# Performance work log

Hardware: AMD Instinct MI355X
Metric: run time of the kernel (lower is better)

## Reference

```python
import jax, jax.numpy as jnp
import numpy as np

TEMPERATURE = 0.07
B, D, NUM_CLASSES = 8192, 256, 100

def setup_inputs() -> dict:
    key = jax.random.key(0)
    kz, kl = jax.random.split(key)
    z = jax.random.normal(kz, (B, D), dtype=jnp.float32)
    z = z / jnp.linalg.norm(z, axis=-1, keepdims=True)  # unit-norm embeddings keep exp(logits/T) finite
    labels = jax.random.randint(kl, (B,), 0, NUM_CLASSES, dtype=jnp.int64)
    return {"z": z, "labels": labels}

def reference(z, labels):
    n = z.shape[0]
    same = labels[:, None] == labels[None, :]              # [B, B] bool
    eye = jnp.eye(n, dtype=bool)
    pos_mask = (same & ~eye).astype(z.dtype)               # positives exclude self
    neg_mask = (~same).astype(z.dtype)                     # mask == 0 entries
    exp_logits = jnp.exp(z @ z.T / TEMPERATURE)            # [B, B]
    sum_neg = jnp.sum(exp_logits * neg_mask, axis=1)       # [B]
    # per positive pair: -log(e_ij / (e_ij + sum_neg_i))
    pair_loss = jnp.log1p(sum_neg[:, None] / exp_logits)   # = -log(e/(e+sn)), stable form
    pos_cnt = jnp.sum(pos_mask, axis=1)                    # [B]
    row_loss = jnp.sum(pair_loss * pos_mask, axis=1) / jnp.maximum(pos_cnt, 1.0)
    valid = (pos_cnt > 0).astype(z.dtype)
    n_valid = jnp.sum(valid)
    loss = jnp.where(n_valid > 0,
                     jnp.sum(row_loss * valid) / jnp.maximum(n_valid, 1.0),
                     jnp.zeros((), z.dtype))
    return loss
```

## Files before the change

kernel.cpp:

```cpp
#include <hip/hip_runtime.h>
#include <hip/hip_bf16.h>


#define BN 8192
#define DD 256
#define INV_T (1.0f / 0.07f)
#define CAPI 256
#define CAP 160

typedef __attribute__((ext_vector_type(8))) __bf16 bf16x8;
typedef __attribute__((ext_vector_type(4))) float f32x4;

typedef const __attribute__((address_space(1))) void gas_void;
typedef __attribute__((address_space(3))) void las_void;

static __device__ __forceinline__ void gld_lds16(const void* g, void* l) {
    __builtin_amdgcn_global_load_lds((gas_void*)g, (las_void*)l, 16, 0, 0);
}

static __device__ __forceinline__ unsigned short f2bf(float f) {
    unsigned int u = __builtin_bit_cast(unsigned int, f);
    u = (u + 0x7FFFu + ((u >> 16) & 1u)) >> 16;
    return (unsigned short)u;
}

__global__ __launch_bounds__(256) void k_prep(const float* __restrict__ z,
                                              unsigned short* __restrict__ zbf,
                                              const int* __restrict__ labels,
                                              int* __restrict__ cls_cnt,
                                              int* __restrict__ cls_idx) {
    const int gid = blockIdx.x * 256 + threadIdx.x;
    const float4* z4 = (const float4*)z;
    float4 v0 = z4[gid * 2 + 0];
    float4 v1 = z4[gid * 2 + 1];
    unsigned short r[8];
    r[0] = f2bf(v0.x); r[1] = f2bf(v0.y); r[2] = f2bf(v0.z); r[3] = f2bf(v0.w);
    r[4] = f2bf(v1.x); r[5] = f2bf(v1.y); r[6] = f2bf(v1.z); r[7] = f2bf(v1.w);
    ((uint4*)zbf)[gid] = *(const uint4*)r;
    if (gid < BN) {
        const int c = labels[gid];
        const int slot = atomicAdd(&cls_cnt[c], 1);
        if (slot < CAPI) cls_idx[c * CAPI + slot] = gid;
    }
}

__global__ __launch_bounds__(512, 2) void k_passA(const unsigned short* __restrict__ zbf,
                                                  float* __restrict__ sn_part) {
    __shared__ char Bb[2][65536];
    __shared__ float sn_lds[128];

    const int tid = threadIdx.x;
    const int w = tid >> 6, lane = tid & 63;
    const int l15 = lane & 15, lk = lane >> 4;
    const int wr = w & 1, wc = w >> 1;
    const int by = blockIdx.x >> 2;
    const int cq = blockIdx.x & 3;
    const int rowbase = by * 128;
    const int colbase = cq * 2048;
    const char* zb = (const char*)zbf;

    auto stage = [&](int buf, int ns) {
        const char* gB = zb + ((size_t)(colbase + ns * 128)) * 512;
        char* lb = Bb[buf];
#pragma unroll
        for (int qq = 0; qq < 8; ++qq) {
            const int s = (qq * 512 + tid) * 16;
            const int col = s >> 9, koff = s & 511;
            gld_lds16(gB + (size_t)col * 512 + (koff ^ ((col & 7) << 4)), lb + s);
        }
    };

    {
        const char* gA = zb + (size_t)rowbase * 512;
#pragma unroll
        for (int qq = 0; qq < 8; ++qq) {
            const int s = (qq * 512 + tid) * 16;
            const int row = s >> 9, koff = s & 511;
            gld_lds16(gA + (size_t)row * 512 + (koff ^ ((row & 7) << 4)),
                      (char*)Bb[0] + s);
        }
    }
    __syncthreads();

    bf16x8 a[4][8];
#pragma unroll
    for (int m = 0; m < 4; ++m) {
        const int row = wr * 64 + m * 16 + l15;
        const int sw = (row & 7) << 4;
#pragma unroll
        for (int kf = 0; kf < 8; ++kf)
            a[m][kf] = *(const bf16x8*)(Bb[0] + row * 512 + ((lk * 16 + kf * 64) ^ sw));
    }
    if (tid < 128) sn_lds[tid] = 0.f;
    float snp[4][4] = {};
    __syncthreads();

    stage(0, 0);
    stage(1, 1);
    asm volatile("s_waitcnt vmcnt(8)" ::: "memory");
    __builtin_amdgcn_s_barrier();
    __builtin_amdgcn_sched_barrier(0);

    for (int ns = 0; ns < 16; ++ns) {
        const int buf = ns & 1;
        const char* bp0 = Bb[buf];
        f32x4 acc[2][4];

#pragma unroll
        for (int n = 0; n < 2; ++n) {
            const int colL = wc * 32 + n * 16 + l15;
            const char* bp = bp0 + (size_t)colL * 512;
            const int sw = (colL & 7) << 4;
            bf16x8 b[8];
#pragma unroll
            for (int kf = 0; kf < 8; ++kf)
                b[kf] = *(const bf16x8*)(bp + ((lk * 16 + kf * 64) ^ sw));
#pragma unroll
            for (int m = 0; m < 4; ++m) acc[n][m] = (f32x4){0.f, 0.f, 0.f, 0.f};
            __builtin_amdgcn_s_setprio(1);
#pragma unroll
            for (int kf = 0; kf < 8; ++kf)
#pragma unroll
                for (int m = 0; m < 4; ++m)
                    acc[n][m] = __builtin_amdgcn_mfma_f32_16x16x32_bf16(a[m][kf], b[kf], acc[n][m], 0, 0, 0);
            __builtin_amdgcn_s_setprio(0);
        }

        __builtin_amdgcn_sched_barrier(0);
        __builtin_amdgcn_s_barrier();
        if (ns + 2 < 16) stage(buf, ns + 2);

#pragma unroll
        for (int n = 0; n < 2; ++n) {
            const int jj = colbase + ns * 128 + wc * 32 + n * 16 + l15;
#pragma unroll
            for (int m = 0; m < 4; ++m) {
                const int ig = rowbase + wr * 64 + m * 16 + lk * 4;
#pragma unroll
                for (int rr = 0; rr < 4; ++rr) {
                    float e = __expf(acc[n][m][rr] * INV_T);
                    if (ig + rr == jj) e = 0.f;
                    snp[m][rr] += e;
                }
            }
        }

        if (ns + 2 < 16) {
            asm volatile("s_waitcnt vmcnt(8)" ::: "memory");
        } else {
            asm volatile("s_waitcnt vmcnt(0)" ::: "memory");
        }
        __builtin_amdgcn_s_barrier();
        __builtin_amdgcn_sched_barrier(0);
    }

#pragma unroll
    for (int m = 0; m < 4; ++m) {
#pragma unroll
        for (int rr = 0; rr < 4; ++rr) {
            float v = snp[m][rr];
            v += __shfl_xor(v, 1, 64);
            v += __shfl_xor(v, 2, 64);
            v += __shfl_xor(v, 4, 64);
            v += __shfl_xor(v, 8, 64);
            if (l15 == 0)
                atomicAdd(&sn_lds[wr * 64 + m * 16 + lk * 4 + rr], v);
        }
    }
    __syncthreads();
    if (tid < 128)
        sn_part[(size_t)cq * BN + rowbase + tid] = sn_lds[tid];
}

__global__ __launch_bounds__(512) void k_passB(const unsigned short* __restrict__ zbf,
                                               const float* __restrict__ sn_part,
                                               const int* __restrict__ cls_cnt,
                                               const int* __restrict__ cls_idx,
                                               float* __restrict__ gacc) {
    __shared__ char Zc[CAP * 512];
    __shared__ int glist[CAP];
    __shared__ float snl[CAP];
    __shared__ float sums[CAP];
    __shared__ float blkL;

    const int c = blockIdx.x;
    const int tid = threadIdx.x;
    const int w = tid >> 6, lane = tid & 63;
    const int l15 = lane & 15, lk = lane >> 4;
    const char* zb = (const char*)zbf;

    const int n_c = min(cls_cnt[c], CAP);
    const int nt = (n_c + 15) >> 4;
    const int rows_p = nt * 16;

    if (tid < CAP) glist[tid] = (tid < n_c) ? cls_idx[c * CAPI + tid] : 0;
    if (tid == 0) blkL = 0.f;
    __syncthreads();

    for (int e2 = w * 2; e2 < rows_p; e2 += 16) {
        const int row = e2 + (lane >> 5);
        const int cb = (lane & 31) * 16;
        gld_lds16(zb + (size_t)glist[row] * 512 + (cb ^ ((row & 7) << 4)),
                  (char*)Zc + e2 * 512);
    }
    __syncthreads();

    for (int mi = w; mi < nt; mi += 8) {
        const int rowA = mi * 16 + l15;
        const int swa = (rowA & 7) << 4;
        bf16x8 a[8];
#pragma unroll
        for (int kf = 0; kf < 8; ++kf)
            a[kf] = *(const bf16x8*)(Zc + rowA * 512 + ((lk * 16 + kf * 64) ^ swa));
        float sp[4] = {};
        for (int nj = 0; nj < nt; ++nj) {
            const int colB = nj * 16 + l15;
            const int swb = (colB & 7) << 4;
            bf16x8 b[8];
#pragma unroll
            for (int kf = 0; kf < 8; ++kf)
                b[kf] = *(const bf16x8*)(Zc + colB * 512 + ((lk * 16 + kf * 64) ^ swb));
            f32x4 acc = {};
#pragma unroll
            for (int kf = 0; kf < 8; ++kf)
                acc = __builtin_amdgcn_mfma_f32_16x16x32_bf16(a[kf], b[kf], acc, 0, 0, 0);
#pragma unroll
            for (int rr = 0; rr < 4; ++rr) {
                const int i = mi * 16 + lk * 4 + rr;
                const float e = __expf(acc[rr] * INV_T);
                sp[rr] += (colB < n_c && i != colB) ? e : 0.f;
            }
        }
#pragma unroll
        for (int rr = 0; rr < 4; ++rr) {
            float v = sp[rr];
            v += __shfl_xor(v, 1, 64);
            v += __shfl_xor(v, 2, 64);
            v += __shfl_xor(v, 4, 64);
            v += __shfl_xor(v, 8, 64);
            if (l15 == 0) sums[mi * 16 + lk * 4 + rr] = v;
        }
    }
    __syncthreads();
    if (tid < CAP)
        snl[tid] = (tid < n_c)
            ? (sn_part[glist[tid]] + sn_part[BN + glist[tid]]
               + sn_part[2 * BN + glist[tid]] + sn_part[3 * BN + glist[tid]]
               - sums[tid])
            : 0.f;
    __syncthreads();

    for (int mi = w; mi < nt; mi += 8) {
        const int rowA = mi * 16 + l15;
        const int swa = (rowA & 7) << 4;
        bf16x8 a[8];
#pragma unroll
        for (int kf = 0; kf < 8; ++kf)
            a[kf] = *(const bf16x8*)(Zc + rowA * 512 + ((lk * 16 + kf * 64) ^ swa));
        float sneg[4];
#pragma unroll
        for (int rr = 0; rr < 4; ++rr) {
            const int i = mi * 16 + lk * 4 + rr;
            sneg[rr] = (i < n_c) ? snl[i] : 0.f;
        }
        float sp[4] = {};
        for (int nj = 0; nj < nt; ++nj) {
            const int colB = nj * 16 + l15;
            const int swb = (colB & 7) << 4;
            bf16x8 b[8];
#pragma unroll
            for (int kf = 0; kf < 8; ++kf)
                b[kf] = *(const bf16x8*)(Zc + colB * 512 + ((lk * 16 + kf * 64) ^ swb));
            f32x4 acc = {};
#pragma unroll
            for (int kf = 0; kf < 8; ++kf)
                acc = __builtin_amdgcn_mfma_f32_16x16x32_bf16(a[kf], b[kf], acc, 0, 0, 0);
#pragma unroll
            for (int rr = 0; rr < 4; ++rr) {
                const int i = mi * 16 + lk * 4 + rr;
                const float t = log1pf(sneg[rr] * __expf(-acc[rr] * INV_T));
                sp[rr] += (colB < n_c && i != colB) ? t : 0.f;
            }
        }
#pragma unroll
        for (int rr = 0; rr < 4; ++rr) {
            float v = sp[rr];
            v += __shfl_xor(v, 1, 64);
            v += __shfl_xor(v, 2, 64);
            v += __shfl_xor(v, 4, 64);
            v += __shfl_xor(v, 8, 64);
            const int i = mi * 16 + lk * 4 + rr;
            if (l15 == 0 && i < n_c && n_c > 1)
                atomicAdd(&blkL, v / (float)(n_c - 1));
        }
    }
    __syncthreads();
    if (tid == 0 && n_c > 1) {
        atomicAdd(&gacc[0], blkL);
        atomicAdd(&gacc[1], (float)n_c);
    }
}

__global__ void k_final(const float* __restrict__ gacc, float* __restrict__ out) {
    if (threadIdx.x == 0) {
        const float L = gacc[0], V = gacc[1];
        out[0] = (V > 0.f) ? L / fmaxf(V, 1.f) : 0.f;
    }
}

extern "C" void kernel_launch(void* const* d_in, const int* in_sizes, int n_in,
                              void* d_out, int out_size, void* d_ws, size_t ws_size,
                              hipStream_t stream) {
    const float* z      = (const float*)d_in[0];
    const int*   labels = (const int*)d_in[1];
    float* out = (float*)d_out;

    char* ws = (char*)d_ws;
    unsigned short* zbf = (unsigned short*)ws;
    size_t off = (size_t)BN * DD * sizeof(unsigned short);
    float* sn_part = (float*)(ws + off);  off += 4 * BN * sizeof(float);
    int*   cls_cnt = (int*)(ws + off);    off += 1024;
    float* gacc    = (float*)(ws + off);  off += 8;
    int*   cls_idx = (int*)(ws + off);    off += 100 * CAPI * sizeof(int);

    hipMemsetAsync(cls_cnt, 0, 1032, stream);
    k_prep  <<<1024, 256, 0, stream>>>(z, zbf, labels, cls_cnt, cls_idx);
    k_passA <<<256, 512, 0, stream>>>(zbf, sn_part);
    k_passB <<<100, 512, 0, stream>>>(zbf, sn_part, cls_cnt, cls_idx, gacc);
    k_final <<<1, 64, 0, stream>>>(gacc, out);
}
```

Before: 85.83 us.

## Pre-swizzle bf16 embeddings into MFMA fragment layout and drop LDS staging

The prep kernel now writes bf16 embeddings in a 16-row fragment-major layout, so pass A can load A and B operands directly from global memory into registers with coalesced 16-byte loads. This removes the LDS double-buffering and barriers, and pass A moves to 512 blocks of 64 rows each. Pass B now reads fp32 z and converts it itself, and caches the within-class exp matrix as bf16 in LDS so the second GEMM and exp are not recomputed. The costs are more global/L2 traffic for B operands per wave, since nothing is shared through LDS, and a little precision lost by storing exp values in bf16.

```diff
diff --git a/kernel.cpp b/kernel.cpp
--- a/kernel.cpp
+++ b/kernel.cpp
@@ -7,25 +7,23 @@
 #define INV_T (1.0f / 0.07f)
 #define CAPI 256
 #define CAP 160
+#define IPAD 164
 
 typedef __attribute__((ext_vector_type(8))) __bf16 bf16x8;
 typedef __attribute__((ext_vector_type(4))) float f32x4;
-
-typedef const __attribute__((address_space(1))) void gas_void;
-typedef __attribute__((address_space(3))) void las_void;
-
-static __device__ __forceinline__ void gld_lds16(const void* g, void* l) {
-    __builtin_amdgcn_global_load_lds((gas_void*)g, (las_void*)l, 16, 0, 0);
-}
 
 static __device__ __forceinline__ unsigned short f2bf(float f) {
     unsigned int u = __builtin_bit_cast(unsigned int, f);
     u = (u + 0x7FFFu + ((u >> 16) & 1u)) >> 16;
     return (unsigned short)u;
 }
+static __device__ __forceinline__ float bf2f(unsigned short s) {
+    unsigned int u = (unsigned int)s << 16;
+    return __builtin_bit_cast(float, u);
+}
 
 __global__ __launch_bounds__(256) void k_prep(const float* __restrict__ z,
-                                              unsigned short* __restrict__ zbf,
+                                              unsigned short* __restrict__ zbf2,
                                               const int* __restrict__ labels,
                                               int* __restrict__ cls_cnt,
                                               int* __restrict__ cls_idx) {
@@ -36,7 +34,9 @@
     unsigned short r[8];
     r[0] = f2bf(v0.x); r[1] = f2bf(v0.y); r[2] = f2bf(v0.z); r[3] = f2bf(v0.w);
     r[4] = f2bf(v1.x); r[5] = f2bf(v1.y); r[6] = f2bf(v1.z); r[7] = f2bf(v1.w);
-    ((uint4*)zbf)[gid] = *(const uint4*)r;
+    const int j = gid >> 5, c5 = gid & 31;
+    const int idx16 = (((j >> 4) * 8 + (c5 >> 2)) * 64) + (c5 & 3) * 16 + (j & 15);
+    ((uint4*)zbf2)[idx16] = *(const uint4*)r;
     if (gid < BN) {
         const int c = labels[gid];
         const int slot = atomicAdd(&cls_cnt[c], 1);
@@ -44,114 +44,66 @@
     }
 }
 
-__global__ __launch_bounds__(512, 2) void k_passA(const unsigned short* __restrict__ zbf,
+__global__ __launch_bounds__(512, 2) void k_passA(const char* __restrict__ zb2,
                                                   float* __restrict__ sn_part) {
-    __shared__ char Bb[2][65536];
-    __shared__ float sn_lds[128];
-
+    __shared__ float sn_lds[64];
     const int tid = threadIdx.x;
     const int w = tid >> 6, lane = tid & 63;
     const int l15 = lane & 15, lk = lane >> 4;
-    const int wr = w & 1, wc = w >> 1;
-    const int by = blockIdx.x >> 2;
+    const int rowbase = (blockIdx.x >> 2) * 64;
     const int cq = blockIdx.x & 3;
-    const int rowbase = by * 128;
-    const int colbase = cq * 2048;
-    const char* zb = (const char*)zbf;
-
-    auto stage = [&](int buf, int ns) {
-        const char* gB = zb + ((size_t)(colbase + ns * 128)) * 512;
-        char* lb = Bb[buf];
-#pragma unroll
-        for (int qq = 0; qq < 8; ++qq) {
-            const int s = (qq * 512 + tid) * 16;
-            const int col = s >> 9, koff = s & 511;
-            gld_lds16(gB + (size_t)col * 512 + (koff ^ ((col & 7) << 4)), lb + s);
-        }
+    const int jt0 = cq * 128 + w * 16;
+
+    if (tid < 64) sn_lds[tid] = 0.f;
+    __syncthreads();
+
+    const int rt0 = rowbase >> 4;
+    bf16x8 a[4][8];
+#pragma unroll
+    for (int m = 0; m < 4; ++m) {
+        const char* p = zb2 + ((size_t)(rt0 + m) * 8192) + lane * 16;
+#pragma unroll
+        for (int kf = 0; kf < 8; ++kf)
+            a[m][kf] = *(const bf16x8*)(p + kf * 1024);
+    }
+
+    float snp[4][4] = {};
+    bf16x8 b0[8], b1[8];
+
+    auto loadB = [&](bf16x8 (&dst)[8], int jt) {
+        const char* p = zb2 + ((size_t)jt * 8192) + lane * 16;
+#pragma unroll
+        for (int kf = 0; kf < 8; ++kf)
+            dst[kf] = *(const bf16x8*)(p + kf * 1024);
     };
-
-    {
-        const char* gA = zb + (size_t)rowbase * 512;
-#pragma unroll
-        for (int qq = 0; qq < 8; ++qq) {
-            const int s = (qq * 512 + tid) * 16;
-            const int row = s >> 9, koff = s & 511;
-            gld_lds16(gA + (size_t)row * 512 + (koff ^ ((row & 7) << 4)),
-                      (char*)Bb[0] + s);
-        }
-    }
-    __syncthreads();
-
-    bf16x8 a[4][8];
-#pragma unroll
-    for (int m = 0; m < 4; ++m) {
-        const int row = wr * 64 + m * 16 + l15;
-        const int sw = (row & 7) << 4;
-#pragma unroll
-        for (int kf = 0; kf < 8; ++kf)
-            a[m][kf] = *(const bf16x8*)(Bb[0] + row * 512 + ((lk * 16 + kf * 64) ^ sw));
-    }
-    if (tid < 128) sn_lds[tid] = 0.f;
-    float snp[4][4] = {};
-    __syncthreads();
-
-    stage(0, 0);
-    stage(1, 1);
-    asm volatile("s_waitcnt vmcnt(8)" ::: "memory");
-    __builtin_amdgcn_s_barrier();
-    __builtin_amdgcn_sched_barrier(0);
-
-    for (int ns = 0; ns < 16; ++ns) {
-        const int buf = ns & 1;
-        const char* bp0 = Bb[buf];
-        f32x4 acc[2][4];
-
-#pragma unroll
-        for (int n = 0; n < 2; ++n) {
-            const int colL = wc * 32 + n * 16 + l15;
-            const char* bp = bp0 + (size_t)colL * 512;
-            const int sw = (colL & 7) << 4;
-            bf16x8 b[8];
-#pragma unroll
-            for (int kf = 0; kf < 8; ++kf)
-                b[kf] = *(const bf16x8*)(bp + ((lk * 16 + kf * 64) ^ sw));
-#pragma unroll
-            for (int m = 0; m < 4; ++m) acc[n][m] = (f32x4){0.f, 0.f, 0.f, 0.f};
-            __builtin_amdgcn_s_setprio(1);
-#pragma unroll
-            for (int kf = 0; kf < 8; ++kf)
-#pragma unroll
-                for (int m = 0; m < 4; ++m)
-                    acc[n][m] = __builtin_amdgcn_mfma_f32_16x16x32_bf16(a[m][kf], b[kf], acc[n][m], 0, 0, 0);
-            __builtin_amdgcn_s_setprio(0);
-        }
-
-        __builtin_amdgcn_sched_barrier(0);
-        __builtin_amdgcn_s_barrier();
-        if (ns + 2 < 16) stage(buf, ns + 2);
-
-#pragma unroll
-        for (int n = 0; n < 2; ++n) {
-            const int jj = colbase + ns * 128 + wc * 32 + n * 16 + l15;
-#pragma unroll
-            for (int m = 0; m < 4; ++m) {
-                const int ig = rowbase + wr * 64 + m * 16 + lk * 4;
-#pragma unroll
-                for (int rr = 0; rr < 4; ++rr) {
-                    float e = __expf(acc[n][m][rr] * INV_T);
-                    if (ig + rr == jj) e = 0.f;
-                    snp[m][rr] += e;
-                }
+    auto computeTile = [&](bf16x8 (&bx)[8], int jt) {
+        f32x4 acc[4] = {};
+        __builtin_amdgcn_s_setprio(1);
+#pragma unroll
+        for (int kf = 0; kf < 8; ++kf)
+#pragma unroll
+            for (int m = 0; m < 4; ++m)
+                acc[m] = __builtin_amdgcn_mfma_f32_16x16x32_bf16(a[m][kf], bx[kf], acc[m], 0, 0, 0);
+        __builtin_amdgcn_s_setprio(0);
+        const int jj = jt * 16 + l15;
+#pragma unroll
+        for (int m = 0; m < 4; ++m) {
+            const int ig = rowbase + m * 16 + lk * 4;
+#pragma unroll
+            for (int rr = 0; rr < 4; ++rr) {
+                float e = __expf(acc[m][rr] * INV_T);
+                if (ig + rr == jj) e = 0.f;
+                snp[m][rr] += e;
             }
         }
-
-        if (ns + 2 < 16) {
-            asm volatile("s_waitcnt vmcnt(8)" ::: "memory");
-        } else {
-            asm volatile("s_waitcnt vmcnt(0)" ::: "memory");
-        }
-        __builtin_amdgcn_s_barrier();
-        __builtin_amdgcn_sched_barrier(0);
+    };
+
+    loadB(b0, jt0);
+    for (int t = 0; t < 16; t += 2) {
+        loadB(b1, jt0 + t + 1);
+        computeTile(b0, jt0 + t);
+        if (t + 2 < 16) loadB(b0, jt0 + t + 2);
+        computeTile(b1, jt0 + t + 1);
     }
 
 #pragma unroll
@@ -164,20 +116,21 @@
             v += __shfl_xor(v, 4, 64);
             v += __shfl_xor(v, 8, 64);
             if (l15 == 0)
-                atomicAdd(&sn_lds[wr * 64 + m * 16 + lk * 4 + rr], v);
-        }
-    }
-    __syncthreads();
-    if (tid < 128)
+                atomicAdd(&sn_lds[m * 16 + lk * 4 + rr], v);
+        }
+    }
+    __syncthreads();
+    if (tid < 64)
         sn_part[(size_t)cq * BN + rowbase + tid] = sn_lds[tid];
 }
 
-__global__ __launch_bounds__(512) void k_passB(const unsigned short* __restrict__ zbf,
+__global__ __launch_bounds__(512) void k_passB(const float* __restrict__ zf,
                                                const float* __restrict__ sn_part,
                                                const int* __restrict__ cls_cnt,
                                                const int* __restrict__ cls_idx,
                                                float* __restrict__ gacc) {
     __shared__ char Zc[CAP * 512];
+    __shared__ unsigned short dmat[CAP * IPAD];
     __shared__ int glist[CAP];
     __shared__ float snl[CAP];
     __shared__ float sums[CAP];
@@ -187,7 +140,6 @@
     const int tid = threadIdx.x;
     const int w = tid >> 6, lane = tid & 63;
     const int l15 = lane & 15, lk = lane >> 4;
-    const char* zb = (const char*)zbf;
 
     const int n_c = min(cls_cnt[c], CAP);
     const int nt = (n_c + 15) >> 4;
@@ -199,9 +151,14 @@
 
     for (int e2 = w * 2; e2 < rows_p; e2 += 16) {
         const int row = e2 + (lane >> 5);
-        const int cb = (lane & 31) * 16;
-        gld_lds16(zb + (size_t)glist[row] * 512 + (cb ^ ((row & 7) << 4)),
-                  (char*)Zc + e2 * 512);
+        const int li = lane & 31;
+        const float* src = zf + (size_t)glist[row] * DD + li * 8;
+        float4 v0 = *(const float4*)(src);
+        float4 v1 = *(const float4*)(src + 4);
+        unsigned short r[8];
+        r[0] = f2bf(v0.x); r[1] = f2bf(v0.y); r[2] = f2bf(v0.z); r[3] = f2bf(v0.w);
+        r[4] = f2bf(v1.x); r[5] = f2bf(v1.y); r[6] = f2bf(v1.z); r[7] = f2bf(v1.w);
+        *(uint4*)(Zc + row * 512 + ((li * 16) ^ ((row & 7) << 4))) = *(const uint4*)r;
     }
     __syncthreads();
 
@@ -224,12 +181,18 @@
 #pragma unroll
             for (int kf = 0; kf < 8; ++kf)
                 acc = __builtin_amdgcn_mfma_f32_16x16x32_bf16(a[kf], b[kf], acc, 0, 0, 0);
+            unsigned short ep[4];
 #pragma unroll
             for (int rr = 0; rr < 4; ++rr) {
                 const int i = mi * 16 + lk * 4 + rr;
                 const float e = __expf(acc[rr] * INV_T);
+                ep[rr] = f2bf(e);
                 sp[rr] += (colB < n_c && i != colB) ? e : 0.f;
             }
+            uint2 uv;
+            uv.x = (unsigned)ep[0] | ((unsigned)ep[1] << 16);
+            uv.y = (unsigned)ep[2] | ((unsigned)ep[3] << 16);
+            *(uint2*)&dmat[colB * IPAD + mi * 16 + lk * 4] = uv;
         }
 #pragma unroll
         for (int rr = 0; rr < 4; ++rr) {
@@ -251,12 +214,6 @@
     __syncthreads();
 
     for (int mi = w; mi < nt; mi += 8) {
-        const int rowA = mi * 16 + l15;
-        const int swa = (rowA & 7) << 4;
-        bf16x8 a[8];
-#pragma unroll
-        for (int kf = 0; kf < 8; ++kf)
-            a[kf] = *(const bf16x8*)(Zc + rowA * 512 + ((lk * 16 + kf * 64) ^ swa));
         float sneg[4];
 #pragma unroll
         for (int rr = 0; rr < 4; ++rr) {
@@ -266,19 +223,16 @@
         float sp[4] = {};
         for (int nj = 0; nj < nt; ++nj) {
             const int colB = nj * 16 + l15;
-            const int swb = (colB & 7) << 4;
-            bf16x8 b[8];
-#pragma unroll
-            for (int kf = 0; kf < 8; ++kf)
-                b[kf] = *(const bf16x8*)(Zc + colB * 512 + ((lk * 16 + kf * 64) ^ swb));
-            f32x4 acc = {};
-#pragma unroll
-            for (int kf = 0; kf < 8; ++kf)
-                acc = __builtin_amdgcn_mfma_f32_16x16x32_bf16(a[kf], b[kf], acc, 0, 0, 0);
+            const uint2 pk = *(const uint2*)&dmat[colB * IPAD + mi * 16 + lk * 4];
+            float ev[4];
+            ev[0] = bf2f((unsigned short)(pk.x & 0xffff));
+            ev[1] = bf2f((unsigned short)(pk.x >> 16));
+            ev[2] = bf2f((unsigned short)(pk.y & 0xffff));
+            ev[3] = bf2f((unsigned short)(pk.y >> 16));
 #pragma unroll
             for (int rr = 0; rr < 4; ++rr) {
                 const int i = mi * 16 + lk * 4 + rr;
-                const float t = log1pf(sneg[rr] * __expf(-acc[rr] * INV_T));
+                const float t = log1pf(sneg[rr] / ev[rr]);
                 sp[rr] += (colB < n_c && i != colB) ? t : 0.f;
             }
         }
@@ -316,7 +270,7 @@
     float* out = (float*)d_out;
 
     char* ws = (char*)d_ws;
-    unsigned short* zbf = (unsigned short*)ws;
+    unsigned short* zbf2 = (unsigned short*)ws;
     size_t off = (size_t)BN * DD * sizeof(unsigned short);
     float* sn_part = (float*)(ws + off);  off += 4 * BN * sizeof(float);
     int*   cls_cnt = (int*)(ws + off);    off += 1024;
@@ -324,8 +278,8 @@
     int*   cls_idx = (int*)(ws + off);    off += 100 * CAPI * sizeof(int);
 
     hipMemsetAsync(cls_cnt, 0, 1032, stream);
-    k_prep  <<<1024, 256, 0, stream>>>(z, zbf, labels, cls_cnt, cls_idx);
-    k_passA <<<256, 512, 0, stream>>>(zbf, sn_part);
-    k_passB <<<100, 512, 0, stream>>>(zbf, sn_part, cls_cnt, cls_idx, gacc);
+    k_prep  <<<1024, 256, 0, stream>>>(z, zbf2, labels, cls_cnt, cls_idx);
+    k_passA <<<512, 512, 0, stream>>>((const char*)zbf2, sn_part);
+    k_passB <<<100, 512, 0, stream>>>(z, sn_part, cls_cnt, cls_idx, gacc);
     k_final <<<1, 64, 0, stream>>>(gacc, out);
 }
```

Result: slower. 87.74 us (+2.2%).
